# Kernel tuning notes

Measured on AMD Instinct MI355X. Metric: run time of the kernel, lower is better.

Reference implementation:

```python
import jax, jax.numpy as jnp
import numpy as np

B, S, H = 32, 1024, 768          # batch, seq_len, bert hidden
E, W, P = 128, 8, 512            # entities/sample, span width, rel pairs/sample
NT, NR = 5, 9                    # entity types, relation types
D1, HEADS1, D2, RD = 128, 2, 64, 32
REL_IN = 2 * D2 + RD + H         # 928


def _layernorm(x, g, b):
    m = x.mean(-1, keepdims=True)
    v = x.var(-1, keepdims=True)
    return (x - m) * jax.lax.rsqrt(v + 1e-5) * g + b


def _gat_dense(x, Wm, a_src, a_dst, bias, concat):
    # Fully-connected entity graph (incl. self-loops, PyG GATConv default).
    Bn, En, _ = x.shape
    Hh, D = a_src.shape
    h = (x @ Wm).reshape(Bn, En, Hh, D)                      # [B,E,h,D]
    s = jnp.einsum('behd,hd->beh', h, a_src)                 # source score
    d = jnp.einsum('behd,hd->beh', h, a_dst)                 # target score
    # edge j->i : e_ij = leaky_relu(s_j + d_i)
    e = jax.nn.leaky_relu(d[:, :, None, :] + s[:, None, :, :], 0.2)  # [B,i,j,h]
    alpha = jax.nn.softmax(e, axis=2)
    o = jnp.einsum('bijh,bjhd->bihd', alpha, h)
    o = o.reshape(Bn, En, Hh * D) if concat else o.mean(axis=2)
    return o + bias


def setup_inputs() -> dict:
    key = jax.random.key(0)
    ks = jax.random.split(key, 20)
    f = lambda k, shape: jax.random.normal(k, shape, jnp.float32) * 0.02
    return dict(
        sequence_output=jax.random.normal(ks[0], (B, S, H), jnp.float32),
        entity_starts=jax.random.randint(ks[1], (B, E), 0, S - W),
        entity_type_ids=jax.random.randint(ks[2], (B, E), 0, NT),
        pair_idx=jax.random.randint(ks[3], (B, P, 2), 0, E),
        rel_type_ids=jax.random.randint(ks[4], (B, P), 0, NR),
        entity_type_emb=f(ks[5], (NT, H)),
        rel_type_emb=f(ks[6], (NR, RD)),
        W1=f(ks[7], (H, HEADS1 * D1)), a_src1=f(ks[8], (HEADS1, D1)),
        a_dst1=f(ks[9], (HEADS1, D1)), b1=jnp.zeros((HEADS1 * D1,), jnp.float32),
        ln1_g=jnp.ones((HEADS1 * D1,), jnp.float32), ln1_b=jnp.zeros((HEADS1 * D1,), jnp.float32),
        W2=f(ks[10], (HEADS1 * D1, D2)), a_src2=f(ks[11], (1, D2)),
        a_dst2=f(ks[12], (1, D2)), b2=jnp.zeros((D2,), jnp.float32),
        ln2_g=jnp.ones((D2,), jnp.float32), ln2_b=jnp.zeros((D2,), jnp.float32),
        Wr1=f(ks[13], (REL_IN, 256)), br1=jnp.zeros((256,), jnp.float32),
        Wr2=f(ks[14], (256, 1)), br2=jnp.zeros((1,), jnp.float32),
    )


def reference(sequence_output, entity_starts, entity_type_ids, pair_idx, rel_type_ids,
              entity_type_emb, rel_type_emb,
              W1, a_src1, a_dst1, b1, ln1_g, ln1_b,
              W2, a_src2, a_dst2, b2, ln2_g, ln2_b,
              Wr1, br1, Wr2, br2):
    bidx = jnp.arange(B)[:, None]
    # --- per-entity attention pooling over span tokens ---
    tok_idx = entity_starts[:, :, None] + jnp.arange(W)            # [B,E,W]
    toks = sequence_output[jnp.arange(B)[:, None, None], tok_idx]  # [B,E,W,H]
    mean = toks.mean(axis=2)                                       # [B,E,H]
    attn = jax.nn.softmax(jnp.einsum('bewh,beh->bew', toks, mean), axis=-1)
    pooled = jnp.einsum('bew,bewh->beh', attn, toks)
    x = pooled + entity_type_emb[entity_type_ids]                  # [B,E,H]
    # --- 2-layer GAT over fully-connected entity graph ---
    x = jax.nn.elu(_layernorm(_gat_dense(x, W1, a_src1, a_dst1, b1, True), ln1_g, ln1_b))
    x = jax.nn.elu(_layernorm(_gat_dense(x, W2, a_src2, a_dst2, b2, False), ln2_g, ln2_b))
    # --- gather-concat relation MLP scoring ---
    cls = sequence_output[:, 0, :]                                 # [B,H]
    x1 = x[bidx, pair_idx[:, :, 0]]                                # [B,P,64]
    x2 = x[bidx, pair_idx[:, :, 1]]
    rel = rel_type_emb[rel_type_ids]                               # [B,P,32]
    pv = jnp.concatenate([x1, x2, rel, jnp.broadcast_to(cls[:, None, :], (B, P, H))], axis=-1)
    scores = (jax.nn.relu(pv @ Wr1 + br1) @ Wr2 + br2)[..., 0]     # [B,P]
    return scores
```

## Files before the change

kernel.cpp:

```cpp
#include <hip/hip_runtime.h>
#include <hip/hip_bf16.h>

#define BB 32
#define SS 1024
#define HHH 768
#define EE 128
#define WW 8
#define PP 512
#define ND1 128
#define NH1 2
#define ND2 64
#define RDD 32

typedef __attribute__((ext_vector_type(8))) short bf16x8;
typedef __attribute__((ext_vector_type(8))) unsigned short us8;
typedef __attribute__((ext_vector_type(4))) float f32x4;

__device__ __forceinline__ unsigned short f2bf(float v) {
    __hip_bfloat16 h = __float2bfloat16(v);
    return *(unsigned short*)&h;
}
__device__ __forceinline__ float bf2f(unsigned short u) {
    unsigned int x = ((unsigned int)u) << 16;
    float f; __builtin_memcpy(&f, &x, 4);
    return f;
}

__global__ __launch_bounds__(256) void pool_kernel(
    const float* __restrict__ seq, const int* __restrict__ starts,
    const int* __restrict__ types, const float* __restrict__ temb,
    const float* __restrict__ br1, float* __restrict__ baseo,
    unsigned short* __restrict__ xout) {
    int be = blockIdx.x;
    int b = be >> 7;
    int tid = threadIdx.x;
    __shared__ float toks[WW][HHH];
    __shared__ float scred[WW];
    __shared__ float attn_s[WW];

    if (be < BB) baseo[(size_t)be * 256 + tid] = br1[tid];

    int start = starts[be];
    const float4* bp4 = (const float4*)(seq + ((size_t)b * SS + start) * HHH);
    for (int idx = tid; idx < WW * (HHH / 4); idx += 256) {
        int w = idx / (HHH / 4), h4 = idx % (HHH / 4);
        float4 v = bp4[(size_t)w * (HHH / 4) + h4];
        toks[w][h4 * 4 + 0] = v.x; toks[w][h4 * 4 + 1] = v.y;
        toks[w][h4 * 4 + 2] = v.z; toks[w][h4 * 4 + 3] = v.w;
    }
    __syncthreads();

    float sc[WW];
#pragma unroll
    for (int w = 0; w < WW; w++) sc[w] = 0.f;
#pragma unroll
    for (int c = 0; c < 3; c++) {
        int h = tid + 256 * c;
        float s = 0.f;
#pragma unroll
        for (int w = 0; w < WW; w++) s += toks[w][h];
        float m = s * (1.0f / WW);
#pragma unroll
        for (int w = 0; w < WW; w++) sc[w] += toks[w][h] * m;
    }
    if (tid < WW) scred[tid] = 0.f;
    __syncthreads();
    int lane = tid & 63;
#pragma unroll
    for (int w = 0; w < WW; w++) {
        float v = sc[w];
        for (int o = 32; o > 0; o >>= 1) v += __shfl_down(v, o, 64);
        if (lane == 0) atomicAdd(&scred[w], v);
    }
    __syncthreads();
    if (tid == 0) {
        float mx = scred[0];
        for (int w = 1; w < WW; w++) mx = fmaxf(mx, scred[w]);
        float ssum = 0.f;
        float a[WW];
        for (int w = 0; w < WW; w++) { a[w] = __expf(scred[w] - mx); ssum += a[w]; }
        float inv = 1.f / ssum;
        for (int w = 0; w < WW; w++) attn_s[w] = a[w] * inv;
    }
    __syncthreads();

    int t = types[be];
    const float* emb = temb + (size_t)t * HHH;
#pragma unroll
    for (int c = 0; c < 3; c++) {
        int h = tid + 256 * c;
        float p = 0.f;
#pragma unroll
        for (int w = 0; w < WW; w++) p += attn_s[w] * toks[w][h];
        xout[(size_t)be * HHH + h] = f2bf(p + emb[h]);
    }
}

__global__ __launch_bounds__(256) void prep_kernel(
    const float* __restrict__ W1, unsigned short* __restrict__ Wt,
    const float* __restrict__ Wr1, unsigned short* __restrict__ Wtr,
    const float* __restrict__ W2, unsigned short* __restrict__ W2t,
    const float* __restrict__ seq, float* __restrict__ baseo) {
    int blk = blockIdx.x;
    int tid = threadIdx.x;
    __shared__ float wbuf[16][256];
    if (blk < 48) {
        int k0 = blk * 16;
        for (int i = tid; i < 16 * 256; i += 256)
            wbuf[i >> 8][i & 255] = W1[(size_t)(k0 + (i >> 8)) * 256 + (i & 255)];
        __syncthreads();
        int n = tid;
        us8 v0, v1;
#pragma unroll
        for (int kk = 0; kk < 8; kk++) v0[kk] = f2bf(wbuf[kk][n]);
#pragma unroll
        for (int kk = 0; kk < 8; kk++) v1[kk] = f2bf(wbuf[8 + kk][n]);
        *(us8*)(Wt + (size_t)n * HHH + k0) = v0;
        *(us8*)(Wt + (size_t)n * HHH + k0 + 8) = v1;
    } else if (blk < 58) {
        int k0 = (blk - 48) * 16;
        for (int i = tid; i < 16 * 256; i += 256)
            wbuf[i >> 8][i & 255] = Wr1[(size_t)(k0 + (i >> 8)) * 256 + (i & 255)];
        __syncthreads();
        int n = tid;
        us8 v0, v1;
#pragma unroll
        for (int kk = 0; kk < 8; kk++) v0[kk] = f2bf(wbuf[kk][n]);
#pragma unroll
        for (int kk = 0; kk < 8; kk++) v1[kk] = f2bf(wbuf[8 + kk][n]);
        *(us8*)(Wtr + (size_t)n * 160 + k0) = v0;
        *(us8*)(Wtr + (size_t)n * 160 + k0 + 8) = v1;
    } else if (blk < 74) {
        int k0 = (blk - 58) * 16;
        for (int i = tid; i < 16 * 64; i += 256)
            wbuf[i >> 6][i & 63] = W2[(size_t)(k0 + (i >> 6)) * 64 + (i & 63)];
        __syncthreads();
        if (tid < 64) {
            int n = tid;
            us8 v0, v1;
#pragma unroll
            for (int kk = 0; kk < 8; kk++) v0[kk] = f2bf(wbuf[kk][n]);
#pragma unroll
            for (int kk = 0; kk < 8; kk++) v1[kk] = f2bf(wbuf[8 + kk][n]);
            *(us8*)(W2t + (size_t)n * 256 + k0) = v0;
            *(us8*)(W2t + (size_t)n * 256 + k0 + 8) = v1;
        }
    } else {
        int pc = blk - 74;
        int kc = pc % 12;
        int b = pc / 12;
        int n = tid;
        __shared__ float cls[64];
        if (n < 64) cls[n] = seq[(size_t)b * SS * HHH + kc * 64 + n];
        __syncthreads();
        float acc = 0.f;
        const float* w = Wr1 + (size_t)(160 + kc * 64) * 256 + n;
#pragma unroll 16
        for (int k = 0; k < 64; k++) acc += cls[k] * w[(size_t)k * 256];
        atomicAdd(&baseo[(size_t)b * 256 + n], acc);
    }
}

__global__ __launch_bounds__(256) void gemm1_mfma_kernel(
    const unsigned short* __restrict__ Xb, const unsigned short* __restrict__ Wt,
    float* __restrict__ C) {
    const int K = HHH;
    int n0 = blockIdx.x * 64;
    int m0 = blockIdx.y * 64;
    int tid = threadIdx.x;
    int wave = tid >> 6, lane = tid & 63;
    int wm = (wave >> 1) * 32, wn = (wave & 1) * 32;

    __shared__ __align__(16) unsigned short As[64][40];
    __shared__ __align__(16) unsigned short Bs[64][40];

    f32x4 acc[2][2] = {};
    int ar = tid >> 2;
    int ac = (tid & 3) * 8;
    int fr = lane & 15;
    int fk = (lane >> 4) * 8;

    for (int k0 = 0; k0 < K; k0 += 32) {
        us8 av = *(const us8*)(Xb + (size_t)(m0 + ar) * K + k0 + ac);
        us8 bv = *(const us8*)(Wt + (size_t)(n0 + ar) * K + k0 + ac);
        *(us8*)(&As[ar][ac]) = av;
        *(us8*)(&Bs[ar][ac]) = bv;
        __syncthreads();

        bf16x8 a0 = *(const bf16x8*)(&As[wm + fr][fk]);
        bf16x8 a1 = *(const bf16x8*)(&As[wm + 16 + fr][fk]);
        bf16x8 b0 = *(const bf16x8*)(&Bs[wn + fr][fk]);
        bf16x8 b1 = *(const bf16x8*)(&Bs[wn + 16 + fr][fk]);

        acc[0][0] = __builtin_amdgcn_mfma_f32_16x16x32_bf16(a0, b0, acc[0][0], 0, 0, 0);
        acc[0][1] = __builtin_amdgcn_mfma_f32_16x16x32_bf16(a0, b1, acc[0][1], 0, 0, 0);
        acc[1][0] = __builtin_amdgcn_mfma_f32_16x16x32_bf16(a1, b0, acc[1][0], 0, 0, 0);
        acc[1][1] = __builtin_amdgcn_mfma_f32_16x16x32_bf16(a1, b1, acc[1][1], 0, 0, 0);
        __syncthreads();
    }

    int crow = (lane >> 4) * 4;
    int ccol = lane & 15;
#pragma unroll
    for (int mi = 0; mi < 2; mi++)
#pragma unroll
        for (int ni = 0; ni < 2; ni++)
#pragma unroll
            for (int r = 0; r < 4; r++)
                C[(size_t)(m0 + wm + mi * 16 + crow + r) * 256 +
                  n0 + wn + ni * 16 + ccol] = acc[mi][ni][r];
}

__global__ __launch_bounds__(256) void gat1_fused_kernel(
    const float* __restrict__ h1, const float* __restrict__ a_src1,
    const float* __restrict__ a_dst1, float* __restrict__ g1pre) {
    int b = blockIdx.x >> 1;
    int h = blockIdx.x & 1;
    int tid = threadIdx.x;
    int wave = tid >> 6, lane = tid & 63;
    int wm = wave * 32;
    int fr = lane & 15;
    int fk = (lane >> 4) * 8;

    __shared__ __align__(16) unsigned short h1T[128][136];
    __shared__ float s_sh[128];
    __shared__ float dd_sh[128];

    {
        int d = tid & 127;
        int mb = (tid >> 7) * 8;
        const float* hsrc = h1 + ((size_t)b * 128) * 256 + h * 128 + d;
#pragma unroll
        for (int m = 0; m < 8; m++) {
            int j0 = (mb + m) * 8;
            us8 pk;
#pragma unroll
            for (int jj = 0; jj < 8; jj++)
                pk[jj] = f2bf(hsrc[(size_t)(j0 + jj) * 256]);
            *(us8*)(&h1T[d][j0]) = pk;
        }
    }
    __syncthreads();

    {
        int j = tid & 127;
        const float* av = (tid < 128) ? (a_src1 + h * 128) : (a_dst1 + h * 128);
        float accd = 0.f;
        for (int d2 = 0; d2 < 128; d2++)
            accd += bf2f(h1T[d2][j]) * av[d2];
        if (tid < 128) s_sh[j] = accd;
        else dd_sh[j] = accd;
    }
    __syncthreads();

    bf16x8 afrag[2][4];
#pragma unroll
    for (int mi = 0; mi < 2; mi++) {
        int i = wm + mi * 16 + fr;
        float dd = dd_sh[i];
        float ev[4][8];
        float mx = -1e30f;
#pragma unroll
        for (int ks = 0; ks < 4; ks++)
#pragma unroll
            for (int jj = 0; jj < 8; jj++) {
                float e = dd + s_sh[ks * 32 + fk + jj];
                e = e >= 0.f ? e : 0.2f * e;
                ev[ks][jj] = e;
                mx = fmaxf(mx, e);
            }
        mx = fmaxf(mx, __shfl_xor(mx, 16, 64));
        mx = fmaxf(mx, __shfl_xor(mx, 32, 64));
        float sm = 0.f;
#pragma unroll
        for (int ks = 0; ks < 4; ks++)
#pragma unroll
            for (int jj = 0; jj < 8; jj++) {
                float e = __expf(ev[ks][jj] - mx);
                ev[ks][jj] = e;
                sm += e;
            }
        sm += __shfl_xor(sm, 16, 64);
        sm += __shfl_xor(sm, 32, 64);
        float inv = 1.f / sm;
#pragma unroll
        for (int ks = 0; ks < 4; ks++) {
            bf16x8 a;
#pragma unroll
            for (int jj = 0; jj < 8; jj++)
                a[jj] = (short)f2bf(ev[ks][jj] * inv);
            afrag[mi][ks] = a;
        }
    }

    f32x4 acc[2][8] = {};
#pragma unroll
    for (int ks = 0; ks < 4; ks++) {
#pragma unroll
        for (int ni = 0; ni < 8; ni++) {
            bf16x8 bv = *(const bf16x8*)(&h1T[ni * 16 + fr][ks * 32 + fk]);
            acc[0][ni] = __builtin_amdgcn_mfma_f32_16x16x32_bf16(
                afrag[0][ks], bv, acc[0][ni], 0, 0, 0);
            acc[1][ni] = __builtin_amdgcn_mfma_f32_16x16x32_bf16(
                afrag[1][ks], bv, acc[1][ni], 0, 0, 0);
        }
    }

    int crow = (lane >> 4) * 4;
    int ccol = lane & 15;
#pragma unroll
    for (int mi = 0; mi < 2; mi++)
#pragma unroll
        for (int ni = 0; ni < 8; ni++)
#pragma unroll
            for (int r = 0; r < 4; r++)
                g1pre[(size_t)(b * 128 + wm + mi * 16 + crow + r) * 256 +
                      h * 128 + ni * 16 + ccol] = acc[mi][ni][r];
}

__global__ __launch_bounds__(256) void ln_elu256b_kernel(
    const float* __restrict__ g1pre, const float* __restrict__ b1,
    const float* __restrict__ gamma, const float* __restrict__ beta,
    unsigned short* __restrict__ g1b) {
    int row = blockIdx.x;
    int tid = threadIdx.x;
    __shared__ float red[4];
    float v = g1pre[(size_t)row * 256 + tid] + b1[tid];
    float s = v;
    for (int o = 32; o > 0; o >>= 1) s += __shfl_down(s, o, 64);
    int lane = tid & 63, wid = tid >> 6;
    if (lane == 0) red[wid] = s;
    __syncthreads();
    float mean = (red[0] + red[1] + red[2] + red[3]) * (1.f / 256.f);
    __syncthreads();
    float dv = v - mean;
    float sq = dv * dv;
    for (int o = 32; o > 0; o >>= 1) sq += __shfl_down(sq, o, 64);
    if (lane == 0) red[wid] = sq;
    __syncthreads();
    float var = (red[0] + red[1] + red[2] + red[3]) * (1.f / 256.f);
    float y = dv * rsqrtf(var + 1e-5f) * gamma[tid] + beta[tid];
    y = y > 0.f ? y : (__expf(y) - 1.f);
    g1b[(size_t)row * 256 + tid] = f2bf(y);
}

__global__ __launch_bounds__(256) void gemm2_mfma_kernel(
    const unsigned short* __restrict__ g1b, const unsigned short* __restrict__ W2t,
    const float* __restrict__ asrc, const float* __restrict__ adst,
    float* __restrict__ h2, float* __restrict__ s2, float* __restrict__ d2) {
    int m0 = blockIdx.x * 64;
    int tid = threadIdx.x;
    int wave = tid >> 6, lane = tid & 63;
    int wm = (wave >> 1) * 32, wn = (wave & 1) * 32;

    __shared__ __align__(16) unsigned short As[64][72];
    __shared__ __align__(16) unsigned short Bs[64][72];
    __shared__ float sdred[64][2][2];

    f32x4 acc[2][2] = {};
    int fr = lane & 15;
    int fk = (lane >> 4) * 8;

    for (int kc = 0; kc < 4; kc++) {
        for (int it = 0; it < 2; it++) {
            int i = tid + it * 256;
            int row = i >> 3, c = i & 7;
            *(us8*)(&As[row][c * 8]) =
                *(const us8*)(g1b + (size_t)(m0 + row) * 256 + kc * 64 + c * 8);
            *(us8*)(&Bs[row][c * 8]) =
                *(const us8*)(W2t + (size_t)row * 256 + kc * 64 + c * 8);
        }
        __syncthreads();
#pragma unroll
        for (int ks = 0; ks < 2; ks++) {
            int kb = ks * 32 + fk;
            bf16x8 a0 = *(const bf16x8*)(&As[wm + fr][kb]);
            bf16x8 a1 = *(const bf16x8*)(&As[wm + 16 + fr][kb]);
            bf16x8 b0 = *(const bf16x8*)(&Bs[wn + fr][kb]);
            bf16x8 b1 = *(const bf16x8*)(&Bs[wn + 16 + fr][kb]);
            acc[0][0] = __builtin_amdgcn_mfma_f32_16x16x32_bf16(a0, b0, acc[0][0], 0, 0, 0);
            acc[0][1] = __builtin_amdgcn_mfma_f32_16x16x32_bf16(a0, b1, acc[0][1], 0, 0, 0);
            acc[1][0] = __builtin_amdgcn_mfma_f32_16x16x32_bf16(a1, b0, acc[1][0], 0, 0, 0);
            acc[1][1] = __builtin_amdgcn_mfma_f32_16x16x32_bf16(a1, b1, acc[1][1], 0, 0, 0);
        }
        __syncthreads();
    }

    int crow = (lane >> 4) * 4;
    int ccol = lane & 15;
    float asv[2], adv[2];
#pragma unroll
    for (int ni = 0; ni < 2; ni++) {
        int n = wn + ni * 16 + ccol;
        asv[ni] = asrc[n];
        adv[ni] = adst[n];
    }
#pragma unroll
    for (int mi = 0; mi < 2; mi++) {
#pragma unroll
        for (int r = 0; r < 4; r++) {
            float sp = 0.f, dp = 0.f;
#pragma unroll
            for (int ni = 0; ni < 2; ni++) {
                float v = acc[mi][ni][r];
                h2[(size_t)(m0 + wm + mi * 16 + crow + r) * 64 +
                   wn + ni * 16 + ccol] = v;
                sp += v * asv[ni];
                dp += v * adv[ni];
            }
            for (int msk = 1; msk < 16; msk <<= 1) {
                sp += __shfl_xor(sp, msk, 64);
                dp += __shfl_xor(dp, msk, 64);
            }
            if ((lane & 15) == 0) {
                int row = wm + mi * 16 + crow + r;
                sdred[row][wn >> 5][0] = sp;
                sdred[row][wn >> 5][1] = dp;
            }
        }
    }
    __syncthreads();
    if (tid < 64 && wave == 0) {
        s2[m0 + tid] = sdred[tid][0][0] + sdred[tid][1][0];
        d2[m0 + tid] = sdred[tid][0][1] + sdred[tid][1][1];
    }
}

__global__ __launch_bounds__(128) void gat2_kernel(
    const float* __restrict__ h2, const float* __restrict__ s2,
    const float* __restrict__ d2, const float* __restrict__ b2v,
    const float* __restrict__ gamma, const float* __restrict__ beta,
    float* __restrict__ x2) {
    int bi = blockIdx.x;
    int b = bi >> 7;
    int tid = threadIdx.x;
    __shared__ float alpha[128];
    __shared__ float red[2];

    float ev = d2[bi] + s2[(size_t)b * 128 + tid];
    ev = ev >= 0.f ? ev : 0.2f * ev;
    float mx = ev;
    for (int o = 32; o > 0; o >>= 1) mx = fmaxf(mx, __shfl_down(mx, o, 64));
    int lane = tid & 63, wid = tid >> 6;
    if (lane == 0) red[wid] = mx;
    __syncthreads();
    mx = fmaxf(red[0], red[1]);
    __syncthreads();
    float ex = __expf(ev - mx);
    float sm = ex;
    for (int o = 32; o > 0; o >>= 1) sm += __shfl_down(sm, o, 64);
    if (lane == 0) red[wid] = sm;
    __syncthreads();
    sm = red[0] + red[1];
    alpha[tid] = ex / sm;
    __syncthreads();

    if (tid < 64) {
        const float* hb = h2 + (size_t)b * 128 * 64 + tid;
        float o = 0.f;
#pragma unroll 8
        for (int j = 0; j < 128; j++) o += alpha[j] * hb[(size_t)j * 64];
        o += b2v[tid];
        float s = o;
        for (int off = 32; off > 0; off >>= 1) s += __shfl_down(s, off, 64);
        s = __shfl(s, 0, 64);
        float mean = s * (1.f / 64.f);
        float dv = o - mean;
        float sq = dv * dv;
        for (int off = 32; off > 0; off >>= 1) sq += __shfl_down(sq, off, 64);
        sq = __shfl(sq, 0, 64);
        float var = sq * (1.f / 64.f);
        float y = dv * rsqrtf(var + 1e-5f) * gamma[tid] + beta[tid];
        y = y > 0.f ? y : (__expf(y) - 1.f);
        x2[(size_t)bi * 64 + tid] = y;
    }
}

__global__ __launch_bounds__(256) void score_mfma_kernel(
    const float* __restrict__ x2, const float* __restrict__ baseo,
    const int* __restrict__ pair_idx, const int* __restrict__ rel_ids,
    const float* __restrict__ rel_emb, const unsigned short* __restrict__ Wtr,
    const float* __restrict__ Wr2, const float* __restrict__ br2,
    float* __restrict__ out) {
    int blk = blockIdx.x;
    int b = blk >> 3;
    int p0 = (blk & 7) * 64;
    int tid = threadIdx.x;
    int wave = tid >> 6, lane = tid & 63;
    int wn = wave * 64;

    __shared__ __align__(16) unsigned short As[64][168];
    __shared__ __align__(16) unsigned short Bs[256][40];
    __shared__ float sred[64][4];
    __shared__ int prs[64][3];

    if (tid < 64) {
        int p = p0 + tid;
        prs[tid][0] = pair_idx[((size_t)b * PP + p) * 2 + 0];
        prs[tid][1] = pair_idx[((size_t)b * PP + p) * 2 + 1];
        prs[tid][2] = rel_ids[(size_t)b * PP + p];
    }
    __syncthreads();
    for (int it = 0; it < 40; it++) {
        int i = tid + it * 256;
        int m = i / 160, k = i % 160;
        float v;
        if (k < 64) v = x2[((size_t)b * EE + prs[m][0]) * 64 + k];
        else if (k < 128) v = x2[((size_t)b * EE + prs[m][1]) * 64 + (k - 64)];
        else v = rel_emb[prs[m][2] * RDD + (k - 128)];
        As[m][k] = f2bf(v);
    }

    f32x4 acc[4][4] = {};
    int fr = lane & 15;
    int fk = (lane >> 4) * 8;

    for (int kc = 0; kc < 5; kc++) {
        for (int it = 0; it < 4; it++) {
            int i = tid + it * 256;
            int n = i >> 2, c = i & 3;
            *(us8*)(&Bs[n][c * 8]) =
                *(const us8*)(Wtr + (size_t)n * 160 + kc * 32 + c * 8);
        }
        __syncthreads();
        bf16x8 a[4], bv[4];
#pragma unroll
        for (int mi = 0; mi < 4; mi++)
            a[mi] = *(const bf16x8*)(&As[mi * 16 + fr][kc * 32 + fk]);
#pragma unroll
        for (int ni = 0; ni < 4; ni++)
            bv[ni] = *(const bf16x8*)(&Bs[wn + ni * 16 + fr][fk]);
#pragma unroll
        for (int mi = 0; mi < 4; mi++)
#pragma unroll
            for (int ni = 0; ni < 4; ni++)
                acc[mi][ni] = __builtin_amdgcn_mfma_f32_16x16x32_bf16(
                    a[mi], bv[ni], acc[mi][ni], 0, 0, 0);
        __syncthreads();
    }

    int crow = (lane >> 4) * 4;
    int ccol = lane & 15;
    float basev[4], w2v[4];
#pragma unroll
    for (int ni = 0; ni < 4; ni++) {
        int n = wn + ni * 16 + ccol;
        basev[ni] = baseo[(size_t)b * 256 + n];
        w2v[ni] = Wr2[n];
    }
#pragma unroll
    for (int mi = 0; mi < 4; mi++) {
#pragma unroll
        for (int r = 0; r < 4; r++) {
            float p = 0.f;
#pragma unroll
            for (int ni = 0; ni < 4; ni++)
                p += fmaxf(acc[mi][ni][r] + basev[ni], 0.f) * w2v[ni];
            for (int msk = 1; msk < 16; msk <<= 1)
                p += __shfl_xor(p, msk, 64);
            if ((lane & 15) == 0)
                sred[mi * 16 + crow + r][wave] = p;
        }
    }
    __syncthreads();
    if (tid < 64) {
        float s = sred[tid][0] + sred[tid][1] + sred[tid][2] + sred[tid][3] + br2[0];
        out[(size_t)b * PP + p0 + tid] = s;
    }
}

extern "C" void kernel_launch(void* const* d_in, const int* in_sizes, int n_in,
                              void* d_out, int out_size, void* d_ws, size_t ws_size,
                              hipStream_t stream) {
    (void)in_sizes; (void)n_in; (void)out_size; (void)ws_size;
    const float* seq      = (const float*)d_in[0];
    const int*   starts   = (const int*)d_in[1];
    const int*   types    = (const int*)d_in[2];
    const int*   pair_idx = (const int*)d_in[3];
    const int*   rel_ids  = (const int*)d_in[4];
    const float* temb     = (const float*)d_in[5];
    const float* remb     = (const float*)d_in[6];
    const float* W1       = (const float*)d_in[7];
    const float* a_src1   = (const float*)d_in[8];
    const float* a_dst1   = (const float*)d_in[9];
    const float* b1       = (const float*)d_in[10];
    const float* ln1_g    = (const float*)d_in[11];
    const float* ln1_b    = (const float*)d_in[12];
    const float* W2       = (const float*)d_in[13];
    const float* a_src2   = (const float*)d_in[14];
    const float* a_dst2   = (const float*)d_in[15];
    const float* b2       = (const float*)d_in[16];
    const float* ln2_g    = (const float*)d_in[17];
    const float* ln2_b    = (const float*)d_in[18];
    const float* Wr1      = (const float*)d_in[19];
    const float* br1      = (const float*)d_in[20];
    const float* Wr2      = (const float*)d_in[21];
    const float* br2      = (const float*)d_in[22];
    float* out = (float*)d_out;

    unsigned short* xb  = (unsigned short*)d_ws;
    unsigned short* Wt  = xb + (size_t)4096 * 768;
    unsigned short* Wtr = Wt + (size_t)256 * 768;
    unsigned short* W2t = Wtr + (size_t)256 * 160;
    unsigned short* g1b = W2t + (size_t)64 * 256;
    float* fbase = (float*)(g1b + (size_t)4096 * 256);
    float* h1    = fbase;
    float* g1pre = h1 + (size_t)4096 * 256;
    float* h2    = g1pre + (size_t)4096 * 256;
    float* s2    = h2 + (size_t)4096 * 64;
    float* d2    = s2 + 4096;
    float* x2    = d2 + 4096;
    float* baseo = x2 + (size_t)4096 * 64;

    pool_kernel<<<BB * EE, 256, 0, stream>>>(seq, starts, types, temb, br1, baseo, xb);
    prep_kernel<<<74 + 12 * 32, 256, 0, stream>>>(W1, Wt, Wr1, Wtr, W2, W2t, seq, baseo);
    gemm1_mfma_kernel<<<dim3(4, 64), 256, 0, stream>>>(xb, Wt, h1);
    gat1_fused_kernel<<<BB * 2, 256, 0, stream>>>(h1, a_src1, a_dst1, g1pre);
    ln_elu256b_kernel<<<BB * EE, 256, 0, stream>>>(g1pre, b1, ln1_g, ln1_b, g1b);
    gemm2_mfma_kernel<<<64, 256, 0, stream>>>(g1b, W2t, a_src2, a_dst2, h2, s2, d2);
    gat2_kernel<<<BB * EE, 128, 0, stream>>>(h2, s2, d2, b2, ln2_g, ln2_b, x2);
    score_mfma_kernel<<<BB * PP / 64, 256, 0, stream>>>(x2, baseo, pair_idx, rel_ids,
                                                        remb, Wtr, Wr2, br2, out);
}
```

Measured before the change: 260.2 us.

## Fuse pooling with prep, fold LayerNorm into GAT kernels, use MFMA for GAT2

Measured after the change: 250.9 us. 1.04x faster.

```diff
diff --git a/kernel.cpp b/kernel.cpp
--- a/kernel.cpp
+++ b/kernel.cpp
@@ -7,13 +7,11 @@
 #define EE 128
 #define WW 8
 #define PP 512
-#define ND1 128
-#define NH1 2
-#define ND2 64
 #define RDD 32
 
 typedef __attribute__((ext_vector_type(8))) short bf16x8;
 typedef __attribute__((ext_vector_type(8))) unsigned short us8;
+typedef __attribute__((ext_vector_type(4))) unsigned short us4;
 typedef __attribute__((ext_vector_type(4))) float f32x4;
 
 __device__ __forceinline__ unsigned short f2bf(float v) {
@@ -26,138 +24,136 @@
     return f;
 }
 
-__global__ __launch_bounds__(256) void pool_kernel(
+__global__ __launch_bounds__(256) void pool_prep_kernel(
     const float* __restrict__ seq, const int* __restrict__ starts,
     const int* __restrict__ types, const float* __restrict__ temb,
-    const float* __restrict__ br1, float* __restrict__ baseo,
-    unsigned short* __restrict__ xout) {
-    int be = blockIdx.x;
-    int b = be >> 7;
-    int tid = threadIdx.x;
-    __shared__ float toks[WW][HHH];
-    __shared__ float scred[WW];
-    __shared__ float attn_s[WW];
-
-    if (be < BB) baseo[(size_t)be * 256 + tid] = br1[tid];
-
-    int start = starts[be];
-    const float4* bp4 = (const float4*)(seq + ((size_t)b * SS + start) * HHH);
-    for (int idx = tid; idx < WW * (HHH / 4); idx += 256) {
-        int w = idx / (HHH / 4), h4 = idx % (HHH / 4);
-        float4 v = bp4[(size_t)w * (HHH / 4) + h4];
-        toks[w][h4 * 4 + 0] = v.x; toks[w][h4 * 4 + 1] = v.y;
-        toks[w][h4 * 4 + 2] = v.z; toks[w][h4 * 4 + 3] = v.w;
-    }
-    __syncthreads();
-
-    float sc[WW];
-#pragma unroll
-    for (int w = 0; w < WW; w++) sc[w] = 0.f;
-#pragma unroll
-    for (int c = 0; c < 3; c++) {
-        int h = tid + 256 * c;
-        float s = 0.f;
-#pragma unroll
-        for (int w = 0; w < WW; w++) s += toks[w][h];
-        float m = s * (1.0f / WW);
-#pragma unroll
-        for (int w = 0; w < WW; w++) sc[w] += toks[w][h] * m;
-    }
-    if (tid < WW) scred[tid] = 0.f;
-    __syncthreads();
-    int lane = tid & 63;
-#pragma unroll
-    for (int w = 0; w < WW; w++) {
-        float v = sc[w];
-        for (int o = 32; o > 0; o >>= 1) v += __shfl_down(v, o, 64);
-        if (lane == 0) atomicAdd(&scred[w], v);
-    }
-    __syncthreads();
-    if (tid == 0) {
-        float mx = scred[0];
-        for (int w = 1; w < WW; w++) mx = fmaxf(mx, scred[w]);
-        float ssum = 0.f;
-        float a[WW];
-        for (int w = 0; w < WW; w++) { a[w] = __expf(scred[w] - mx); ssum += a[w]; }
-        float inv = 1.f / ssum;
-        for (int w = 0; w < WW; w++) attn_s[w] = a[w] * inv;
-    }
-    __syncthreads();
-
-    int t = types[be];
-    const float* emb = temb + (size_t)t * HHH;
-#pragma unroll
-    for (int c = 0; c < 3; c++) {
-        int h = tid + 256 * c;
-        float p = 0.f;
-#pragma unroll
-        for (int w = 0; w < WW; w++) p += attn_s[w] * toks[w][h];
-        xout[(size_t)be * HHH + h] = f2bf(p + emb[h]);
-    }
-}
-
-__global__ __launch_bounds__(256) void prep_kernel(
+    unsigned short* __restrict__ xout,
     const float* __restrict__ W1, unsigned short* __restrict__ Wt,
     const float* __restrict__ Wr1, unsigned short* __restrict__ Wtr,
     const float* __restrict__ W2, unsigned short* __restrict__ W2t,
-    const float* __restrict__ seq, float* __restrict__ baseo) {
-    int blk = blockIdx.x;
+    const float* __restrict__ remb, unsigned short* __restrict__ rembb,
+    float* __restrict__ basep) {
     int tid = threadIdx.x;
-    __shared__ float wbuf[16][256];
+    __shared__ float sbuf[WW * HHH];
+    __shared__ float scred[WW];
+    __shared__ float attn_s[WW];
+
+    if (blockIdx.x < BB * EE) {
+        int be = blockIdx.x;
+        int b = be >> 7;
+        int start = starts[be];
+        const float4* bp4 = (const float4*)(seq + ((size_t)b * SS + start) * HHH);
+        for (int idx = tid; idx < WW * (HHH / 4); idx += 256) {
+            int w = idx / (HHH / 4), h4 = idx % (HHH / 4);
+            float4 v = bp4[(size_t)w * (HHH / 4) + h4];
+            sbuf[w * HHH + h4 * 4 + 0] = v.x; sbuf[w * HHH + h4 * 4 + 1] = v.y;
+            sbuf[w * HHH + h4 * 4 + 2] = v.z; sbuf[w * HHH + h4 * 4 + 3] = v.w;
+        }
+        __syncthreads();
+
+        float sc[WW];
+#pragma unroll
+        for (int w = 0; w < WW; w++) sc[w] = 0.f;
+#pragma unroll
+        for (int c = 0; c < 3; c++) {
+            int h = tid + 256 * c;
+            float s = 0.f;
+#pragma unroll
+            for (int w = 0; w < WW; w++) s += sbuf[w * HHH + h];
+            float m = s * (1.0f / WW);
+#pragma unroll
+            for (int w = 0; w < WW; w++) sc[w] += sbuf[w * HHH + h] * m;
+        }
+        if (tid < WW) scred[tid] = 0.f;
+        __syncthreads();
+        int lane = tid & 63;
+#pragma unroll
+        for (int w = 0; w < WW; w++) {
+            float v = sc[w];
+            for (int o = 32; o > 0; o >>= 1) v += __shfl_down(v, o, 64);
+            if (lane == 0) atomicAdd(&scred[w], v);
+        }
+        __syncthreads();
+        if (tid == 0) {
+            float mx = scred[0];
+            for (int w = 1; w < WW; w++) mx = fmaxf(mx, scred[w]);
+            float ssum = 0.f;
+            float a[WW];
+            for (int w = 0; w < WW; w++) { a[w] = __expf(scred[w] - mx); ssum += a[w]; }
+            float inv = 1.f / ssum;
+            for (int w = 0; w < WW; w++) attn_s[w] = a[w] * inv;
+        }
+        __syncthreads();
+
+        int t = types[be];
+        const float* emb = temb + (size_t)t * HHH;
+#pragma unroll
+        for (int c = 0; c < 3; c++) {
+            int h = tid + 256 * c;
+            float p = 0.f;
+#pragma unroll
+            for (int w = 0; w < WW; w++) p += attn_s[w] * sbuf[w * HHH + h];
+            xout[(size_t)be * HHH + h] = f2bf(p + emb[h]);
+        }
+        return;
+    }
+
+    int blk = blockIdx.x - BB * EE;
     if (blk < 48) {
         int k0 = blk * 16;
         for (int i = tid; i < 16 * 256; i += 256)
-            wbuf[i >> 8][i & 255] = W1[(size_t)(k0 + (i >> 8)) * 256 + (i & 255)];
+            sbuf[i] = W1[(size_t)(k0 + (i >> 8)) * 256 + (i & 255)];
         __syncthreads();
         int n = tid;
         us8 v0, v1;
 #pragma unroll
-        for (int kk = 0; kk < 8; kk++) v0[kk] = f2bf(wbuf[kk][n]);
-#pragma unroll
-        for (int kk = 0; kk < 8; kk++) v1[kk] = f2bf(wbuf[8 + kk][n]);
+        for (int kk = 0; kk < 8; kk++) v0[kk] = f2bf(sbuf[kk * 256 + n]);
+#pragma unroll
+        for (int kk = 0; kk < 8; kk++) v1[kk] = f2bf(sbuf[(8 + kk) * 256 + n]);
         *(us8*)(Wt + (size_t)n * HHH + k0) = v0;
         *(us8*)(Wt + (size_t)n * HHH + k0 + 8) = v1;
     } else if (blk < 58) {
         int k0 = (blk - 48) * 16;
         for (int i = tid; i < 16 * 256; i += 256)
-            wbuf[i >> 8][i & 255] = Wr1[(size_t)(k0 + (i >> 8)) * 256 + (i & 255)];
+            sbuf[i] = Wr1[(size_t)(k0 + (i >> 8)) * 256 + (i & 255)];
         __syncthreads();
         int n = tid;
         us8 v0, v1;
 #pragma unroll
-        for (int kk = 0; kk < 8; kk++) v0[kk] = f2bf(wbuf[kk][n]);
-#pragma unroll
-        for (int kk = 0; kk < 8; kk++) v1[kk] = f2bf(wbuf[8 + kk][n]);
+        for (int kk = 0; kk < 8; kk++) v0[kk] = f2bf(sbuf[kk * 256 + n]);
+#pragma unroll
+        for (int kk = 0; kk < 8; kk++) v1[kk] = f2bf(sbuf[(8 + kk) * 256 + n]);
         *(us8*)(Wtr + (size_t)n * 160 + k0) = v0;
         *(us8*)(Wtr + (size_t)n * 160 + k0 + 8) = v1;
     } else if (blk < 74) {
         int k0 = (blk - 58) * 16;
         for (int i = tid; i < 16 * 64; i += 256)
-            wbuf[i >> 6][i & 63] = W2[(size_t)(k0 + (i >> 6)) * 64 + (i & 63)];
+            sbuf[(i >> 6) * 64 + (i & 63)] = W2[(size_t)(k0 + (i >> 6)) * 64 + (i & 63)];
         __syncthreads();
         if (tid < 64) {
             int n = tid;
             us8 v0, v1;
 #pragma unroll
-            for (int kk = 0; kk < 8; kk++) v0[kk] = f2bf(wbuf[kk][n]);
-#pragma unroll
-            for (int kk = 0; kk < 8; kk++) v1[kk] = f2bf(wbuf[8 + kk][n]);
+            for (int kk = 0; kk < 8; kk++) v0[kk] = f2bf(sbuf[kk * 64 + n]);
+#pragma unroll
+            for (int kk = 0; kk < 8; kk++) v1[kk] = f2bf(sbuf[(8 + kk) * 64 + n]);
             *(us8*)(W2t + (size_t)n * 256 + k0) = v0;
             *(us8*)(W2t + (size_t)n * 256 + k0 + 8) = v1;
         }
+    } else if (blk == 74) {
+        for (int i = tid; i < 9 * RDD; i += 256) rembb[i] = f2bf(remb[i]);
     } else {
-        int pc = blk - 74;
+        int pc = blk - 75;
         int kc = pc % 12;
         int b = pc / 12;
         int n = tid;
-        __shared__ float cls[64];
-        if (n < 64) cls[n] = seq[(size_t)b * SS * HHH + kc * 64 + n];
+        if (n < 64) sbuf[4096 + n] = seq[(size_t)b * SS * HHH + kc * 64 + n];
         __syncthreads();
         float acc = 0.f;
         const float* w = Wr1 + (size_t)(160 + kc * 64) * 256 + n;
 #pragma unroll 16
-        for (int k = 0; k < 64; k++) acc += cls[k] * w[(size_t)k * 256];
-        atomicAdd(&baseo[(size_t)b * 256 + n], acc);
+        for (int k = 0; k < 64; k++) acc += sbuf[4096 + k] * w[(size_t)k * 256];
+        basep[((size_t)kc * 32 + b) * 256 + n] = acc;
     }
 }
 
@@ -213,135 +209,147 @@
 
 __global__ __launch_bounds__(256) void gat1_fused_kernel(
     const float* __restrict__ h1, const float* __restrict__ a_src1,
-    const float* __restrict__ a_dst1, float* __restrict__ g1pre) {
-    int b = blockIdx.x >> 1;
-    int h = blockIdx.x & 1;
+    const float* __restrict__ a_dst1, const float* __restrict__ b1,
+    const float* __restrict__ gamma, const float* __restrict__ beta,
+    unsigned short* __restrict__ g1b) {
+    int b = blockIdx.x;
     int tid = threadIdx.x;
     int wave = tid >> 6, lane = tid & 63;
     int wm = wave * 32;
     int fr = lane & 15;
     int fk = (lane >> 4) * 8;
 
-    __shared__ __align__(16) unsigned short h1T[128][136];
-    __shared__ float s_sh[128];
-    __shared__ float dd_sh[128];
+    __shared__ __align__(16) unsigned short h1T[2][128][136];
+    __shared__ float ssh[2][128];
+    __shared__ float dsh[2][128];
 
     {
-        int d = tid & 127;
-        int mb = (tid >> 7) * 8;
-        const float* hsrc = h1 + ((size_t)b * 128) * 256 + h * 128 + d;
-#pragma unroll
-        for (int m = 0; m < 8; m++) {
-            int j0 = (mb + m) * 8;
-            us8 pk;
-#pragma unroll
-            for (int jj = 0; jj < 8; jj++)
-                pk[jj] = f2bf(hsrc[(size_t)(j0 + jj) * 256]);
-            *(us8*)(&h1T[d][j0]) = pk;
+        const float4* src4 = (const float4*)(h1 + (size_t)b * 128 * 256);
+        for (int it = 0; it < 32; it++) {
+            int i4 = tid + it * 256;
+            int j = i4 >> 6;
+            int c4 = i4 & 63;
+            float4 v = src4[(size_t)j * 64 + c4];
+            int d = c4 * 4;
+            int hh = d >> 7, dl = d & 127;
+            h1T[hh][dl + 0][j] = f2bf(v.x);
+            h1T[hh][dl + 1][j] = f2bf(v.y);
+            h1T[hh][dl + 2][j] = f2bf(v.z);
+            h1T[hh][dl + 3][j] = f2bf(v.w);
         }
     }
     __syncthreads();
 
     {
-        int j = tid & 127;
-        const float* av = (tid < 128) ? (a_src1 + h * 128) : (a_dst1 + h * 128);
-        float accd = 0.f;
-        for (int d2 = 0; d2 < 128; d2++)
-            accd += bf2f(h1T[d2][j]) * av[d2];
-        if (tid < 128) s_sh[j] = accd;
-        else dd_sh[j] = accd;
+        int hh = tid >> 7, j = tid & 127;
+        const float* as = a_src1 + hh * 128;
+        const float* ad = a_dst1 + hh * 128;
+        float s_ = 0.f, d_ = 0.f;
+        for (int d2 = 0; d2 < 128; d2++) {
+            float hv = bf2f(h1T[hh][d2][j]);
+            s_ += hv * as[d2];
+            d_ += hv * ad[d2];
+        }
+        ssh[hh][j] = s_;
+        dsh[hh][j] = d_;
     }
     __syncthreads();
 
-    bf16x8 afrag[2][4];
-#pragma unroll
-    for (int mi = 0; mi < 2; mi++) {
-        int i = wm + mi * 16 + fr;
-        float dd = dd_sh[i];
-        float ev[4][8];
-        float mx = -1e30f;
-#pragma unroll
-        for (int ks = 0; ks < 4; ks++)
-#pragma unroll
-            for (int jj = 0; jj < 8; jj++) {
-                float e = dd + s_sh[ks * 32 + fk + jj];
-                e = e >= 0.f ? e : 0.2f * e;
-                ev[ks][jj] = e;
-                mx = fmaxf(mx, e);
-            }
-        mx = fmaxf(mx, __shfl_xor(mx, 16, 64));
-        mx = fmaxf(mx, __shfl_xor(mx, 32, 64));
-        float sm = 0.f;
-#pragma unroll
-        for (int ks = 0; ks < 4; ks++)
-#pragma unroll
-            for (int jj = 0; jj < 8; jj++) {
-                float e = __expf(ev[ks][jj] - mx);
-                ev[ks][jj] = e;
-                sm += e;
-            }
-        sm += __shfl_xor(sm, 16, 64);
-        sm += __shfl_xor(sm, 32, 64);
-        float inv = 1.f / sm;
-#pragma unroll
-        for (int ks = 0; ks < 4; ks++) {
-            bf16x8 a;
-#pragma unroll
-            for (int jj = 0; jj < 8; jj++)
-                a[jj] = (short)f2bf(ev[ks][jj] * inv);
-            afrag[mi][ks] = a;
-        }
-    }
-
-    f32x4 acc[2][8] = {};
-#pragma unroll
-    for (int ks = 0; ks < 4; ks++) {
-#pragma unroll
-        for (int ni = 0; ni < 8; ni++) {
-            bf16x8 bv = *(const bf16x8*)(&h1T[ni * 16 + fr][ks * 32 + fk]);
+    bf16x8 afrag[2][2][4];
+#pragma unroll
+    for (int hh = 0; hh < 2; hh++)
+#pragma unroll
+        for (int mi = 0; mi < 2; mi++) {
+            int i = wm + mi * 16 + fr;
+            float dd = dsh[hh][i];
+            float ev[4][8];
+            float mx = -1e30f;
+#pragma unroll
+            for (int ks = 0; ks < 4; ks++)
+#pragma unroll
+                for (int jj = 0; jj < 8; jj++) {
+                    float e = dd + ssh[hh][ks * 32 + fk + jj];
+                    e = e >= 0.f ? e : 0.2f * e;
+                    ev[ks][jj] = e;
+                    mx = fmaxf(mx, e);
+                }
+            mx = fmaxf(mx, __shfl_xor(mx, 16, 64));
+            mx = fmaxf(mx, __shfl_xor(mx, 32, 64));
+            float sm = 0.f;
+#pragma unroll
+            for (int ks = 0; ks < 4; ks++)
+#pragma unroll
+                for (int jj = 0; jj < 8; jj++) {
+                    float e = __expf(ev[ks][jj] - mx);
+                    ev[ks][jj] = e;
+                    sm += e;
+                }
+            sm += __shfl_xor(sm, 16, 64);
+            sm += __shfl_xor(sm, 32, 64);
+            float inv = 1.f / sm;
+#pragma unroll
+            for (int ks = 0; ks < 4; ks++) {
+                bf16x8 a;
+#pragma unroll
+                for (int jj = 0; jj < 8; jj++)
+                    a[jj] = (short)f2bf(ev[ks][jj] * inv);
+                afrag[hh][mi][ks] = a;
+            }
+        }
+
+    f32x4 acc[2][16] = {};
+#pragma unroll
+    for (int ks = 0; ks < 4; ks++)
+#pragma unroll
+        for (int ni = 0; ni < 16; ni++) {
+            int hh = ni >> 3;
+            bf16x8 bv = *(const bf16x8*)(&h1T[hh][(ni & 7) * 16 + fr][ks * 32 + fk]);
             acc[0][ni] = __builtin_amdgcn_mfma_f32_16x16x32_bf16(
-                afrag[0][ks], bv, acc[0][ni], 0, 0, 0);
+                afrag[hh][0][ks], bv, acc[0][ni], 0, 0, 0);
             acc[1][ni] = __builtin_amdgcn_mfma_f32_16x16x32_bf16(
-                afrag[1][ks], bv, acc[1][ni], 0, 0, 0);
-        }
-    }
+                afrag[hh][1][ks], bv, acc[1][ni], 0, 0, 0);
+        }
 
     int crow = (lane >> 4) * 4;
     int ccol = lane & 15;
+    float bv_[16], gv[16], bev[16];
+#pragma unroll
+    for (int ni = 0; ni < 16; ni++) {
+        int d = ni * 16 + ccol;
+        bv_[ni] = b1[d]; gv[ni] = gamma[d]; bev[ni] = beta[d];
+    }
 #pragma unroll
     for (int mi = 0; mi < 2; mi++)
 #pragma unroll
-        for (int ni = 0; ni < 8; ni++)
-#pragma unroll
-            for (int r = 0; r < 4; r++)
-                g1pre[(size_t)(b * 128 + wm + mi * 16 + crow + r) * 256 +
-                      h * 128 + ni * 16 + ccol] = acc[mi][ni][r];
-}
-
-__global__ __launch_bounds__(256) void ln_elu256b_kernel(
-    const float* __restrict__ g1pre, const float* __restrict__ b1,
-    const float* __restrict__ gamma, const float* __restrict__ beta,
-    unsigned short* __restrict__ g1b) {
-    int row = blockIdx.x;
-    int tid = threadIdx.x;
-    __shared__ float red[4];
-    float v = g1pre[(size_t)row * 256 + tid] + b1[tid];
-    float s = v;
-    for (int o = 32; o > 0; o >>= 1) s += __shfl_down(s, o, 64);
-    int lane = tid & 63, wid = tid >> 6;
-    if (lane == 0) red[wid] = s;
-    __syncthreads();
-    float mean = (red[0] + red[1] + red[2] + red[3]) * (1.f / 256.f);
-    __syncthreads();
-    float dv = v - mean;
-    float sq = dv * dv;
-    for (int o = 32; o > 0; o >>= 1) sq += __shfl_down(sq, o, 64);
-    if (lane == 0) red[wid] = sq;
-    __syncthreads();
-    float var = (red[0] + red[1] + red[2] + red[3]) * (1.f / 256.f);
-    float y = dv * rsqrtf(var + 1e-5f) * gamma[tid] + beta[tid];
-    y = y > 0.f ? y : (__expf(y) - 1.f);
-    g1b[(size_t)row * 256 + tid] = f2bf(y);
+        for (int r = 0; r < 4; r++) {
+            float v[16];
+            float s = 0.f;
+#pragma unroll
+            for (int ni = 0; ni < 16; ni++) {
+                v[ni] = acc[mi][ni][r] + bv_[ni];
+                s += v[ni];
+            }
+            s += __shfl_xor(s, 1, 64); s += __shfl_xor(s, 2, 64);
+            s += __shfl_xor(s, 4, 64); s += __shfl_xor(s, 8, 64);
+            float mean = s * (1.f / 256.f);
+            float sq = 0.f;
+#pragma unroll
+            for (int ni = 0; ni < 16; ni++) {
+                float dv = v[ni] - mean;
+                sq += dv * dv;
+            }
+            sq += __shfl_xor(sq, 1, 64); sq += __shfl_xor(sq, 2, 64);
+            sq += __shfl_xor(sq, 4, 64); sq += __shfl_xor(sq, 8, 64);
+            float rs = rsqrtf(sq * (1.f / 256.f) + 1e-5f);
+            int i = wm + mi * 16 + crow + r;
+            unsigned short* dst = g1b + (size_t)(b * 128 + i) * 256;
+#pragma unroll
+            for (int ni = 0; ni < 16; ni++) {
+                float y = (v[ni] - mean) * rs * gv[ni] + bev[ni];
+                y = y > 0.f ? y : (__expf(y) - 1.f);
+                dst[ni * 16 + ccol] = f2bf(y);
+            }
+        }
 }
 
 __global__ __launch_bounds__(256) void gemm2_mfma_kernel(
@@ -426,60 +434,139 @@
     }
 }
 
-__global__ __launch_bounds__(128) void gat2_kernel(
+__global__ __launch_bounds__(256) void gat2_fused_kernel(
     const float* __restrict__ h2, const float* __restrict__ s2,
     const float* __restrict__ d2, const float* __restrict__ b2v,
     const float* __restrict__ gamma, const float* __restrict__ beta,
-    float* __restrict__ x2) {
-    int bi = blockIdx.x;
-    int b = bi >> 7;
+    unsigned short* __restrict__ x2b) {
+    int b = blockIdx.x;
     int tid = threadIdx.x;
-    __shared__ float alpha[128];
-    __shared__ float red[2];
-
-    float ev = d2[bi] + s2[(size_t)b * 128 + tid];
-    ev = ev >= 0.f ? ev : 0.2f * ev;
-    float mx = ev;
-    for (int o = 32; o > 0; o >>= 1) mx = fmaxf(mx, __shfl_down(mx, o, 64));
-    int lane = tid & 63, wid = tid >> 6;
-    if (lane == 0) red[wid] = mx;
+    int wave = tid >> 6, lane = tid & 63;
+    int wm = wave * 32;
+    int fr = lane & 15;
+    int fk = (lane >> 4) * 8;
+
+    __shared__ __align__(16) unsigned short h2T[64][136];
+    __shared__ float ssh[128];
+    __shared__ float dsh[128];
+
+    {
+        const float4* src4 = (const float4*)(h2 + (size_t)b * 128 * 64);
+        for (int it = 0; it < 8; it++) {
+            int i4 = tid + it * 256;
+            int j = i4 >> 4;
+            int c4 = i4 & 15;
+            float4 v = src4[(size_t)j * 16 + c4];
+            int d = c4 * 4;
+            h2T[d + 0][j] = f2bf(v.x);
+            h2T[d + 1][j] = f2bf(v.y);
+            h2T[d + 2][j] = f2bf(v.z);
+            h2T[d + 3][j] = f2bf(v.w);
+        }
+        if (tid < 128) ssh[tid] = s2[(size_t)b * 128 + tid];
+        else dsh[tid - 128] = d2[(size_t)b * 128 + (tid - 128)];
+    }
     __syncthreads();
-    mx = fmaxf(red[0], red[1]);
-    __syncthreads();
-    float ex = __expf(ev - mx);
-    float sm = ex;
-    for (int o = 32; o > 0; o >>= 1) sm += __shfl_down(sm, o, 64);
-    if (lane == 0) red[wid] = sm;
-    __syncthreads();
-    sm = red[0] + red[1];
-    alpha[tid] = ex / sm;
-    __syncthreads();
-
-    if (tid < 64) {
-        const float* hb = h2 + (size_t)b * 128 * 64 + tid;
-        float o = 0.f;
-#pragma unroll 8
-        for (int j = 0; j < 128; j++) o += alpha[j] * hb[(size_t)j * 64];
-        o += b2v[tid];
-        float s = o;
-        for (int off = 32; off > 0; off >>= 1) s += __shfl_down(s, off, 64);
-        s = __shfl(s, 0, 64);
-        float mean = s * (1.f / 64.f);
-        float dv = o - mean;
-        float sq = dv * dv;
-        for (int off = 32; off > 0; off >>= 1) sq += __shfl_down(sq, off, 64);
-        sq = __shfl(sq, 0, 64);
-        float var = sq * (1.f / 64.f);
-        float y = dv * rsqrtf(var + 1e-5f) * gamma[tid] + beta[tid];
-        y = y > 0.f ? y : (__expf(y) - 1.f);
-        x2[(size_t)bi * 64 + tid] = y;
-    }
+
+    bf16x8 afrag[2][4];
+#pragma unroll
+    for (int mi = 0; mi < 2; mi++) {
+        int i = wm + mi * 16 + fr;
+        float dd = dsh[i];
+        float ev[4][8];
+        float mx = -1e30f;
+#pragma unroll
+        for (int ks = 0; ks < 4; ks++)
+#pragma unroll
+            for (int jj = 0; jj < 8; jj++) {
+                float e = dd + ssh[ks * 32 + fk + jj];
+                e = e >= 0.f ? e : 0.2f * e;
+                ev[ks][jj] = e;
+                mx = fmaxf(mx, e);
+            }
+        mx = fmaxf(mx, __shfl_xor(mx, 16, 64));
+        mx = fmaxf(mx, __shfl_xor(mx, 32, 64));
+        float sm = 0.f;
+#pragma unroll
+        for (int ks = 0; ks < 4; ks++)
+#pragma unroll
+            for (int jj = 0; jj < 8; jj++) {
+                float e = __expf(ev[ks][jj] - mx);
+                ev[ks][jj] = e;
+                sm += e;
+            }
+        sm += __shfl_xor(sm, 16, 64);
+        sm += __shfl_xor(sm, 32, 64);
+        float inv = 1.f / sm;
+#pragma unroll
+        for (int ks = 0; ks < 4; ks++) {
+            bf16x8 a;
+#pragma unroll
+            for (int jj = 0; jj < 8; jj++)
+                a[jj] = (short)f2bf(ev[ks][jj] * inv);
+            afrag[mi][ks] = a;
+        }
+    }
+
+    f32x4 acc[2][4] = {};
+#pragma unroll
+    for (int ks = 0; ks < 4; ks++)
+#pragma unroll
+        for (int ni = 0; ni < 4; ni++) {
+            bf16x8 bv = *(const bf16x8*)(&h2T[ni * 16 + fr][ks * 32 + fk]);
+            acc[0][ni] = __builtin_amdgcn_mfma_f32_16x16x32_bf16(
+                afrag[0][ks], bv, acc[0][ni], 0, 0, 0);
+            acc[1][ni] = __builtin_amdgcn_mfma_f32_16x16x32_bf16(
+                afrag[1][ks], bv, acc[1][ni], 0, 0, 0);
+        }
+
+    int crow = (lane >> 4) * 4;
+    int ccol = lane & 15;
+    float bv_[4], gv[4], bev[4];
+#pragma unroll
+    for (int ni = 0; ni < 4; ni++) {
+        int d = ni * 16 + ccol;
+        bv_[ni] = b2v[d]; gv[ni] = gamma[d]; bev[ni] = beta[d];
+    }
+#pragma unroll
+    for (int mi = 0; mi < 2; mi++)
+#pragma unroll
+        for (int r = 0; r < 4; r++) {
+            float v[4];
+            float s = 0.f;
+#pragma unroll
+            for (int ni = 0; ni < 4; ni++) {
+                v[ni] = acc[mi][ni][r] + bv_[ni];
+                s += v[ni];
+            }
+            s += __shfl_xor(s, 1, 64); s += __shfl_xor(s, 2, 64);
+            s += __shfl_xor(s, 4, 64); s += __shfl_xor(s, 8, 64);
+            float mean = s * (1.f / 64.f);
+            float sq = 0.f;
+#pragma unroll
+            for (int ni = 0; ni < 4; ni++) {
+                float dv = v[ni] - mean;
+                sq += dv * dv;
+            }
+            sq += __shfl_xor(sq, 1, 64); sq += __shfl_xor(sq, 2, 64);
+            sq += __shfl_xor(sq, 4, 64); sq += __shfl_xor(sq, 8, 64);
+            float rs = rsqrtf(sq * (1.f / 64.f) + 1e-5f);
+            int i = wm + mi * 16 + crow + r;
+            unsigned short* dst = x2b + (size_t)(b * 128 + i) * 64;
+#pragma unroll
+            for (int ni = 0; ni < 4; ni++) {
+                float y = (v[ni] - mean) * rs * gv[ni] + bev[ni];
+                y = y > 0.f ? y : (__expf(y) - 1.f);
+                dst[ni * 16 + ccol] = f2bf(y);
+            }
+        }
 }
 
 __global__ __launch_bounds__(256) void score_mfma_kernel(
-    const float* __restrict__ x2, const float* __restrict__ baseo,
+    const unsigned short* __restrict__ x2b, const float* __restrict__ basep,
+    const float* __restrict__ br1,
     const int* __restrict__ pair_idx, const int* __restrict__ rel_ids,
-    const float* __restrict__ rel_emb, const unsigned short* __restrict__ Wtr,
+    const unsigned short* __restrict__ rembb, const unsigned short* __restrict__ Wtr,
     const float* __restrict__ Wr2, const float* __restrict__ br2,
     float* __restrict__ out) {
     int blk = blockIdx.x;
@@ -501,14 +588,18 @@
         prs[tid][2] = rel_ids[(size_t)b * PP + p];
     }
     __syncthreads();
-    for (int it = 0; it < 40; it++) {
-        int i = tid + it * 256;
-        int m = i / 160, k = i % 160;
-        float v;
-        if (k < 64) v = x2[((size_t)b * EE + prs[m][0]) * 64 + k];
-        else if (k < 128) v = x2[((size_t)b * EE + prs[m][1]) * 64 + (k - 64)];
-        else v = rel_emb[prs[m][2] * RDD + (k - 128)];
-        As[m][k] = f2bf(v);
+    for (int it = 0; it < 10; it++) {
+        int idx = tid + it * 256;
+        int m = idx / 40, c = idx % 40;
+        int k0 = c * 4;
+        us4 v;
+        if (k0 < 64)
+            v = *(const us4*)(x2b + ((size_t)b * EE + prs[m][0]) * 64 + k0);
+        else if (k0 < 128)
+            v = *(const us4*)(x2b + ((size_t)b * EE + prs[m][1]) * 64 + (k0 - 64));
+        else
+            v = *(const us4*)(rembb + prs[m][2] * RDD + (k0 - 128));
+        *(us4*)(&As[m][k0]) = v;
     }
 
     f32x4 acc[4][4] = {};
@@ -545,7 +636,11 @@
 #pragma unroll
     for (int ni = 0; ni < 4; ni++) {
         int n = wn + ni * 16 + ccol;
-        basev[ni] = baseo[(size_t)b * 256 + n];
+        float bb = br1[n];
+#pragma unroll
+        for (int kc = 0; kc < 12; kc++)
+            bb += basep[((size_t)kc * 32 + b) * 256 + n];
+        basev[ni] = bb;
         w2v[ni] = Wr2[n];
     }
 #pragma unroll
@@ -598,27 +693,27 @@
     const float* br2      = (const float*)d_in[22];
     float* out = (float*)d_out;
 
-    unsigned short* xb  = (unsigned short*)d_ws;
-    unsigned short* Wt  = xb + (size_t)4096 * 768;
-    unsigned short* Wtr = Wt + (size_t)256 * 768;
-    unsigned short* W2t = Wtr + (size_t)256 * 160;
-    unsigned short* g1b = W2t + (size_t)64 * 256;
-    float* fbase = (float*)(g1b + (size_t)4096 * 256);
+    unsigned short* xb    = (unsigned short*)d_ws;
+    unsigned short* Wt    = xb + (size_t)4096 * 768;
+    unsigned short* Wtr   = Wt + (size_t)256 * 768;
+    unsigned short* W2t   = Wtr + (size_t)256 * 160;
+    unsigned short* rembb = W2t + (size_t)64 * 256;
+    unsigned short* g1b   = rembb + 512;
+    unsigned short* x2b   = g1b + (size_t)4096 * 256;
+    float* fbase = (float*)(x2b + (size_t)4096 * 64);
     float* h1    = fbase;
-    float* g1pre = h1 + (size_t)4096 * 256;
-    float* h2    = g1pre + (size_t)4096 * 256;
+    float* h2    = h1 + (size_t)4096 * 256;
     float* s2    = h2 + (size_t)4096 * 64;
     float* d2    = s2 + 4096;
-    float* x2    = d2 + 4096;
-    float* baseo = x2 + (size_t)4096 * 64;
-
-    pool_kernel<<<BB * EE, 256, 0, stream>>>(seq, starts, types, temb, br1, baseo, xb);
-    prep_kernel<<<74 + 12 * 32, 256, 0, stream>>>(W1, Wt, Wr1, Wtr, W2, W2t, seq, baseo);
+    float* basep = d2 + 4096;
+
+    pool_prep_kernel<<<BB * EE + 75 + 12 * 32, 256, 0, stream>>>(
+        seq, starts, types, temb, xb, W1, Wt, Wr1, Wtr, W2, W2t, remb, rembb, basep);
     gemm1_mfma_kernel<<<dim3(4, 64), 256, 0, stream>>>(xb, Wt, h1);
-    gat1_fused_kernel<<<BB * 2, 256, 0, stream>>>(h1, a_src1, a_dst1, g1pre);
-    ln_elu256b_kernel<<<BB * EE, 256, 0, stream>>>(g1pre, b1, ln1_g, ln1_b, g1b);
+    gat1_fused_kernel<<<BB, 256, 0, stream>>>(h1, a_src1, a_dst1, b1, ln1_g, ln1_b, g1b);
     gemm2_mfma_kernel<<<64, 256, 0, stream>>>(g1b, W2t, a_src2, a_dst2, h2, s2, d2);
-    gat2_kernel<<<BB * EE, 128, 0, stream>>>(h2, s2, d2, b2, ln2_g, ln2_b, x2);
-    score_mfma_kernel<<<BB * PP / 64, 256, 0, stream>>>(x2, baseo, pair_idx, rel_ids,
-                                                        remb, Wtr, Wr2, br2, out);
-}
+    gat2_fused_kernel<<<BB, 256, 0, stream>>>(h2, s2, d2, b2, ln2_g, ln2_b, x2b);
+    score_mfma_kernel<<<BB * PP / 64, 256, 0, stream>>>(x2b, basep, br1, pair_idx,
+                                                        rel_ids, rembb, Wtr, Wr2,
+                                                        br2, out);
+}
```
